# Kernel optimization log

Measured on AMD Instinct MI355X. Metric: run time of the kernel, lower is better.

The kernel has to match this reference:

```python
import jax, jax.numpy as jnp
import numpy as np

B, N, DIM = 4, 1024, 1024
HEADS, DIM_HEAD = 16, 64
ROT = 32
NUM_NULL = 2
EPS = 1e-5


def rotate_half(t):
    t1, t2 = jnp.split(t, 2, axis=-1)
    return jnp.concatenate((-t2, t1), axis=-1)


def apply_rope(t, freqs):
    # t: [..., n, rot]; freqs: [>=n, rot]
    f = freqs[-t.shape[-2]:, :]
    return t * jnp.cos(f) + rotate_half(t) * jnp.sin(f)


def layernorm(x, g, b):
    mu = jnp.mean(x, axis=-1, keepdims=True)
    var = jnp.var(x, axis=-1, keepdims=True)
    return (x - mu) * jax.lax.rsqrt(var + EPS) * g + b


def setup_inputs() -> dict:
    key = jax.random.key(0)
    ks = jax.random.split(key, 8)
    inner = HEADS * DIM_HEAD
    return {
        "x": jax.random.normal(ks[0], (B, N, DIM), jnp.float32),
        "mask": jnp.ones((B, N), dtype=bool),
        "freqs": jax.random.normal(ks[1], (N, ROT), jnp.float32),
        "ln_g": jnp.ones((DIM,), jnp.float32),
        "ln_b": jnp.zeros((DIM,), jnp.float32),
        "W_q": jax.random.normal(ks[2], (DIM, inner), jnp.float32) * (DIM ** -0.5),
        "W_kv": jax.random.normal(ks[3], (DIM, 2 * DIM_HEAD), jnp.float32) * (DIM ** -0.5),
        "W_out": jax.random.normal(ks[4], (inner, DIM), jnp.float32) * (inner ** -0.5),
        "null_kv": jax.random.normal(ks[5], (2, NUM_NULL, DIM_HEAD), jnp.float32),
    }


def reference(x, mask, freqs, ln_g, ln_b, W_q, W_kv, W_out, null_kv):
    b, n, _ = x.shape
    xn = layernorm(x, ln_g, ln_b)
    q = xn @ W_q                       # [b, n, h*d]
    kv = xn @ W_kv                     # [b, n, 2d]
    k, v = jnp.split(kv, 2, axis=-1)   # each [b, n, d] (multi-query)
    q = q.reshape(b, n, HEADS, DIM_HEAD).transpose(0, 2, 1, 3)  # [b, h, n, d]

    # partial rotary on first ROT dims of q, k, v (xpos_scale=None -> scale 1)
    ql, qr = q[..., :ROT], q[..., ROT:]
    kl, kr = k[..., :ROT], k[..., ROT:]
    vl, vr = v[..., :ROT], v[..., ROT:]
    q = jnp.concatenate((apply_rope(ql, freqs), qr), axis=-1)
    k = jnp.concatenate((apply_rope(kl, freqs), kr), axis=-1)
    v = jnp.concatenate((apply_rope(vl, freqs), vr), axis=-1)

    # prepend null k/v
    null_k = jnp.broadcast_to(null_kv[0], (b, NUM_NULL, DIM_HEAD))
    null_v = jnp.broadcast_to(null_kv[1], (b, NUM_NULL, DIM_HEAD))
    k = jnp.concatenate((null_k, k), axis=-2)  # [b, j, d]
    v = jnp.concatenate((null_v, v), axis=-2)
    m = jnp.concatenate((jnp.ones((b, NUM_NULL), bool), mask), axis=-1)  # [b, j]

    i, j = q.shape[-2], k.shape[-2]
    scale = DIM_HEAD ** -0.5
    sim = jnp.einsum('bhid,bjd->bhij', q, k) * scale
    neg = -jnp.finfo(sim.dtype).max
    sim = jnp.where(m[:, None, None, :], sim, neg)
    causal_mask = jnp.triu(jnp.ones((i, j), bool), k=j - i + 1)
    sim = jnp.where(causal_mask, neg, sim)
    attn = jax.nn.softmax(sim, axis=-1)
    out = jnp.einsum('bhij,bjd->bhid', attn, v)
    out = out.transpose(0, 2, 1, 3).reshape(b, n, HEADS * DIM_HEAD)
    return out @ W_out
```

## Files before the change

### kernel.cpp

```cpp
#include <hip/hip_runtime.h>
#include <hip/hip_bf16.h>

typedef __bf16 bf16;
typedef __bf16 bf16x8 __attribute__((ext_vector_type(8)));
typedef float  f32x4  __attribute__((ext_vector_type(4)));

#define SCL 0.18033688011112042f

__device__ __forceinline__ void gl2lds16(const bf16* g, bf16* l) {
    __builtin_amdgcn_global_load_lds(
        (const __attribute__((address_space(1))) unsigned int*)g,
        (__attribute__((address_space(3))) unsigned int*)l, 16, 0, 0);
}

__global__ __launch_bounds__(256) void setup_kernel(
    const float* __restrict__ x, const float* __restrict__ g, const float* __restrict__ b,
    bf16* __restrict__ xn, const float* __restrict__ W_q, const float* __restrict__ W_kv,
    const float* __restrict__ W_out, bf16* __restrict__ wcomb, bf16* __restrict__ wot,
    const float* __restrict__ freqs, const float* __restrict__ nullkv,
    float2* __restrict__ cs, bf16* __restrict__ knull, bf16* __restrict__ vtn) {
    int blk = blockIdx.x, t = threadIdx.x;
    if (blk < 4096) {
        int row = blk;
        float4 v = ((const float4*)(x + (size_t)row * 1024))[t];
        float f0 = v.x, f1 = v.y, f2 = v.z, f3 = v.w;
        float s  = f0 + f1 + f2 + f3;
        float ss = f0 * f0 + f1 * f1 + f2 * f2 + f3 * f3;
#pragma unroll
        for (int off = 32; off; off >>= 1) {
            s  += __shfl_xor(s, off);
            ss += __shfl_xor(ss, off);
        }
        __shared__ float rs[4], rss[4];
        int wave = t >> 6, lane = t & 63;
        if (lane == 0) { rs[wave] = s; rss[wave] = ss; }
        __syncthreads();
        s  = rs[0] + rs[1] + rs[2] + rs[3];
        ss = rss[0] + rss[1] + rss[2] + rss[3];
        float mu  = s * (1.0f / 1024.0f);
        float inv = rsqrtf(ss * (1.0f / 1024.0f) - mu * mu + 1e-5f);
        float4 gv = ((const float4*)g)[t], bv = ((const float4*)b)[t];
        float o0 = (f0 - mu) * inv * gv.x + bv.x;
        float o1 = (f1 - mu) * inv * gv.y + bv.y;
        float o2 = (f2 - mu) * inv * gv.z + bv.z;
        float o3 = (f3 - mu) * inv * gv.w + bv.w;
        __align__(8) bf16 ob[4] = {(bf16)o0, (bf16)o1, (bf16)o2, (bf16)o3};
        ((uint2*)(xn + (size_t)row * 1024))[t] = *(uint2*)ob;
    } else if (blk < 6272) {
        const float* src;
        bf16* dst;
        int R = 1024, C, bx, by;
        if (blk < 5120) {
            src = W_q; dst = wcomb; C = 1024;
            int i = blk - 4096; bx = i & 31; by = i >> 5;
        } else if (blk < 5248) {
            src = W_kv; dst = wcomb + 1024 * 1024; C = 128;
            int i = blk - 5120; bx = i & 3; by = i >> 2;
        } else {
            src = W_out; dst = wot; C = 1024;
            int i = blk - 5248; bx = i & 31; by = i >> 5;
        }
        __shared__ bf16 tile[32][33];
        int tx = t & 31, ty = t >> 5;
        int c0 = bx * 32, r0 = by * 32;
#pragma unroll
        for (int i = 0; i < 4; ++i)
            tile[ty + 8 * i][tx] = (bf16)src[(size_t)(r0 + ty + 8 * i) * C + c0 + tx];
        __syncthreads();
#pragma unroll
        for (int i = 0; i < 4; ++i)
            dst[(size_t)(c0 + ty + 8 * i) * R + r0 + tx] = tile[tx][ty + 8 * i];
    } else if (blk < 6400) {
        int idx = (blk - 6272) * 256 + t;
        float f = freqs[idx];
        cs[idx] = make_float2(cosf(f), sinf(f));
    } else if (blk == 6400) {
        for (int i = t; i < 4 * 62 * 64; i += 256) {
            int bb = i / (62 * 64), rem = i % (62 * 64);
            int r = rem / 64, d = rem % 64;
            knull[((size_t)bb * 1088 + 1026 + r) * 64 + d] = (bf16)0.f;
            vtn[((size_t)(bb * 64 + d)) * 1088 + 1026 + r] = (bf16)0.f;
        }
    } else {
        for (int i = t; i < 4 * 2 * 64; i += 256) {
            int bb = i / 128, rem = i % 128;
            int j = rem / 64, d = rem % 64;
            knull[((size_t)bb * 1088 + j) * 64 + d] = (bf16)(nullkv[j * 64 + d] * SCL);
            vtn[((size_t)(bb * 64 + d)) * 1088 + j] = (bf16)nullkv[128 + j * 64 + d];
        }
    }
}

template <int MODE, typename OutT>
__global__ __launch_bounds__(256) void gemm_glds(const bf16* __restrict__ A,
                                                 const bf16* __restrict__ Bt,
                                                 OutT* __restrict__ C, int K,
                                                 const float2* __restrict__ cs,
                                                 bf16* __restrict__ kout,
                                                 bf16* __restrict__ vout) {
    __shared__ __align__(16) bf16 As[64 * 64];
    __shared__ __align__(16) bf16 Bs[128 * 64];
    const int t = threadIdx.x;
    const int wave = t >> 6, lane = t & 63;
    const int wm = wave >> 1, wn = wave & 1;
    const int r16 = lane & 15, g = lane >> 4;
    const int m0 = blockIdx.x * 64, n0 = blockIdx.y * 128;

    int aRow[2], aOff[2], aLds[2], bRow[4], bOff[4], bLds[4];
#pragma unroll
    for (int j = 0; j < 2; ++j) {
        int c = t + 256 * j, row = c >> 3, p = c & 7;
        aRow[j] = row; aOff[j] = (p ^ (row & 7)) * 8; aLds[j] = c * 8;
    }
#pragma unroll
    for (int j = 0; j < 4; ++j) {
        int c = t + 256 * j, row = c >> 3, p = c & 7;
        bRow[j] = row; bOff[j] = (p ^ (row & 7)) * 8; bLds[j] = c * 8;
    }
    int offA[2][2], offB[2][4];
#pragma unroll
    for (int s = 0; s < 2; ++s) {
#pragma unroll
        for (int i = 0; i < 2; ++i) {
            int rA = wm * 32 + i * 16 + r16;
            offA[s][i] = rA * 64 + (((g + 4 * s) ^ (rA & 7)) * 8);
        }
#pragma unroll
        for (int i = 0; i < 4; ++i) {
            int rB = wn * 64 + i * 16 + r16;
            offB[s][i] = rB * 64 + (((g + 4 * s) ^ (rB & 7)) * 8);
        }
    }

    f32x4 acc[2][4] = {};
    for (int k0 = 0; k0 < K; k0 += 64) {
#pragma unroll
        for (int j = 0; j < 2; ++j)
            gl2lds16(A + (size_t)(m0 + aRow[j]) * K + k0 + aOff[j], As + aLds[j]);
#pragma unroll
        for (int j = 0; j < 4; ++j)
            gl2lds16(Bt + (size_t)(n0 + bRow[j]) * K + k0 + bOff[j], Bs + bLds[j]);
        __syncthreads();
#pragma unroll
        for (int s = 0; s < 2; ++s) {
            bf16x8 af[2], bfr[4];
#pragma unroll
            for (int mi = 0; mi < 2; ++mi) af[mi] = *(const bf16x8*)(As + offA[s][mi]);
#pragma unroll
            for (int ni = 0; ni < 4; ++ni) bfr[ni] = *(const bf16x8*)(Bs + offB[s][ni]);
#pragma unroll
            for (int mi = 0; mi < 2; ++mi)
#pragma unroll
                for (int ni = 0; ni < 4; ++ni)
                    acc[mi][ni] = __builtin_amdgcn_mfma_f32_16x16x32_bf16(
                        af[mi], bfr[ni], acc[mi][ni], 0, 0, 0);
        }
        __syncthreads();
    }
    if constexpr (MODE == 0) {
#pragma unroll
        for (int mi = 0; mi < 2; ++mi)
#pragma unroll
            for (int ni = 0; ni < 4; ++ni)
#pragma unroll
                for (int q2 = 0; q2 < 4; ++q2) {
                    int rr = m0 + wm * 32 + mi * 16 + g * 4 + q2;
                    int ccol = n0 + wn * 64 + ni * 16 + r16;
                    C[(size_t)rr * 1024 + ccol] = (OutT)acc[mi][ni][q2];
                }
    } else {
        bool isq = blockIdx.y < 8;
#pragma unroll
        for (int mi = 0; mi < 2; ++mi)
#pragma unroll
            for (int q2 = 0; q2 < 4; ++q2) {
                int rr = m0 + wm * 32 + mi * 16 + g * 4 + q2;
                int n = rr & 1023, bb = rr >> 10;
                const float2* csr = cs + n * 32;
                float2 c0 = csr[r16], c1 = csr[r16 + 16];
                float t0 = acc[mi][0][q2], t1 = acc[mi][1][q2];
                float t2 = acc[mi][2][q2], t3 = acc[mi][3][q2];
                float o0 = t0 * c0.x - t1 * c0.y;
                float o1 = t1 * c1.x + t0 * c1.y;
                if (isq) {
                    size_t rb = (size_t)rr * 1024 + n0 + wn * 64 + r16;
                    C[rb]      = (OutT)o0;
                    C[rb + 16] = (OutT)o1;
                    C[rb + 32] = (OutT)t2;
                    C[rb + 48] = (OutT)t3;
                } else {
                    if (wn == 0) {
                        bf16* kr = kout + ((size_t)bb * 1088 + n + 2) * 64 + r16;
                        kr[0]  = (bf16)(o0 * SCL);
                        kr[16] = (bf16)(o1 * SCL);
                        kr[32] = (bf16)(t2 * SCL);
                        kr[48] = (bf16)(t3 * SCL);
                    } else {
                        bf16* vr = vout + ((size_t)bb * 64 + r16) * 1088 + n + 2;
                        vr[0]         = (bf16)o0;
                        vr[16 * 1088] = (bf16)o1;
                        vr[32 * 1088] = (bf16)t2;
                        vr[48 * 1088] = (bf16)t3;
                    }
                }
            }
    }
}

__global__ __launch_bounds__(256) void attn_mfma(const bf16* __restrict__ knull,
                                                 const bf16* __restrict__ vtn,
                                                 const bf16* __restrict__ q,
                                                 bf16* __restrict__ out) {
    __shared__ __align__(16) bf16 k_s[2][64 * 64];
    __shared__ __align__(16) bf16 vt_s[2][64 * 64];
    __shared__ __align__(16) bf16 p_s[4][16 * 64];
    const int blk = blockIdx.x;
    const int qt = 15 - (blk >> 6);
    const int bh = blk & 63;
    const int b = bh >> 4, h = bh & 15;
    const int r0 = qt * 64;
    const int t = threadIdx.x, wave = t >> 6, lane = t & 63;
    const int lr = lane & 15, lg = lane >> 4;

    const int sj = t >> 3;
    const bf16* kgp = knull + ((size_t)b * 1088 + sj) * 64 + (t & 7) * 8;
    const bf16* vgp = vtn + ((size_t)(b * 64 + sj)) * 1088 + (t & 7) * 8;
    const int so0 = sj * 64 + (((t & 7) ^ (sj & 7)) * 8);
    const int so1 = so0 + 32 * 64;

#define ISSUE(K0, K1, V0, V1, KB) {                                   \
        int j0_ = (KB) * 64;                                          \
        K0 = *(const uint4*)(kgp + (size_t)j0_ * 64);                 \
        K1 = *(const uint4*)(kgp + (size_t)(j0_ + 32) * 64);          \
        V0 = *(const uint4*)(vgp + j0_);                              \
        V1 = *(const uint4*)(vgp + 32 * 1088 + j0_); }
#define COMMIT(BUF, K0, K1, V0, V1) {                                 \
        *(uint4*)(k_s[BUF] + so0) = K0; *(uint4*)(k_s[BUF] + so1) = K1; \
        *(uint4*)(vt_s[BUF] + so0) = V0; *(uint4*)(vt_s[BUF] + so1) = V1; }

    const int qrow = r0 + wave * 16 + lr;
    const bf16* qp = q + (size_t)(b * 1024 + qrow) * 1024 + h * 64;
    bf16x8 qf0 = *(const bf16x8*)(qp + lg * 8);
    bf16x8 qf1 = *(const bf16x8*)(qp + 32 + lg * 8);

    float m = -3.0e38f, l = 0.f;
    f32x4 O[4] = {};
    const int nkb = qt + 2;
    uint4 kA0, kA1, vA0, vA1, kB0, kB1, vB0, vB1;
    ISSUE(kA0, kA1, vA0, vA1, 0);

    for (int kb = 0; kb < nkb; ++kb) {
        if ((kb & 1) == 0) {
            COMMIT(0, kA0, kA1, vA0, vA1);
            if (kb + 1 < nkb) ISSUE(kB0, kB1, vB0, vB1, kb + 1);
        } else {
            COMMIT(1, kB0, kB1, vB0, vB1);
            if (kb + 1 < nkb) ISSUE(kA0, kA1, vA0, vA1, kb + 1);
        }
        __syncthreads();
        const bf16* ks = k_s[kb & 1];
        const bf16* vs = vt_s[kb & 1];

        if (kb * 64 <= r0 + wave * 16 + 17) {
            f32x4 sc[4];
#pragma unroll
            for (int kt = 0; kt < 4; ++kt) {
                int krow = kt * 16 + lr, sw = lr & 7;
                bf16x8 kf0 = *(const bf16x8*)(ks + krow * 64 + ((lg ^ sw) * 8));
                bf16x8 kf1 = *(const bf16x8*)(ks + krow * 64 + (((4 + lg) ^ sw) * 8));
                sc[kt] = __builtin_amdgcn_mfma_f32_16x16x32_bf16(
                    kf0, qf0, (f32x4){0.f, 0.f, 0.f, 0.f}, 0, 0, 0);
                sc[kt] = __builtin_amdgcn_mfma_f32_16x16x32_bf16(kf1, qf1, sc[kt], 0, 0, 0);
            }
            float pv_[4][4];
            float smax = -3.0e38f;
            bool domask = (kb * 64 + 63 > r0 + wave * 16 + 2);
            if (domask) {
#pragma unroll
                for (int kt = 0; kt < 4; ++kt)
#pragma unroll
                    for (int r = 0; r < 4; ++r) {
                        float s = sc[kt][r];
                        int gkey = kb * 64 + kt * 16 + lg * 4 + r;
                        if (gkey > qrow + 2) s = -3.0e38f;
                        pv_[kt][r] = s;
                        smax = fmaxf(smax, s);
                    }
            } else {
#pragma unroll
                for (int kt = 0; kt < 4; ++kt)
#pragma unroll
                    for (int r = 0; r < 4; ++r) {
                        float s = sc[kt][r];
                        pv_[kt][r] = s;
                        smax = fmaxf(smax, s);
                    }
            }
            smax = fmaxf(smax, __shfl_xor(smax, 16));
            smax = fmaxf(smax, __shfl_xor(smax, 32));
            float mnew = fmaxf(m, smax);
            float corr = exp2f(m - mnew);
            float ps = 0.f;
#pragma unroll
            for (int kt = 0; kt < 4; ++kt)
#pragma unroll
                for (int r = 0; r < 4; ++r) {
                    float p = exp2f(pv_[kt][r] - mnew);
                    pv_[kt][r] = p;
                    ps += p;
                }
            ps += __shfl_xor(ps, 16);
            ps += __shfl_xor(ps, 32);
            l = l * corr + ps;
            m = mnew;
            bf16* pw = p_s[wave];
#pragma unroll
            for (int kt = 0; kt < 4; ++kt) {
                __align__(8) bf16 pk[4] = {(bf16)pv_[kt][0], (bf16)pv_[kt][1],
                                           (bf16)pv_[kt][2], (bf16)pv_[kt][3]};
                int ch = (2 * kt + (lg >> 1)) ^ (lr & 7);
                *(uint2*)((char*)pw + lr * 128 + ch * 16 + (lg & 1) * 8) = *(const uint2*)pk;
            }
            asm volatile("" ::: "memory");
            float corr4[4];
#pragma unroll
            for (int r = 0; r < 4; ++r) corr4[r] = __shfl(corr, lg * 4 + r);
            bf16x8 af0 = *(const bf16x8*)(pw + lr * 64 + ((lg ^ (lr & 7)) * 8));
            bf16x8 af1 = *(const bf16x8*)(pw + lr * 64 + (((4 + lg) ^ (lr & 7)) * 8));
#pragma unroll
            for (int nt = 0; nt < 4; ++nt) {
#pragma unroll
                for (int r = 0; r < 4; ++r) O[nt][r] *= corr4[r];
                int vrow = nt * 16 + lr, sw = lr & 7;
                bf16x8 vf0 = *(const bf16x8*)(vs + vrow * 64 + ((lg ^ sw) * 8));
                bf16x8 vf1 = *(const bf16x8*)(vs + vrow * 64 + (((4 + lg) ^ sw) * 8));
                O[nt] = __builtin_amdgcn_mfma_f32_16x16x32_bf16(af0, vf0, O[nt], 0, 0, 0);
                O[nt] = __builtin_amdgcn_mfma_f32_16x16x32_bf16(af1, vf1, O[nt], 0, 0, 0);
            }
        }
    }
#undef ISSUE
#undef COMMIT
    float l4[4];
#pragma unroll
    for (int r = 0; r < 4; ++r) l4[r] = __shfl(l, lg * 4 + r);
#pragma unroll
    for (int nt = 0; nt < 4; ++nt)
#pragma unroll
        for (int r = 0; r < 4; ++r) {
            int qr = r0 + wave * 16 + 4 * lg + r;
            out[(size_t)(b * 1024 + qr) * 1024 + h * 64 + nt * 16 + lr] =
                (bf16)(O[nt][r] / l4[r]);
        }
}

extern "C" void kernel_launch(void* const* d_in, const int* in_sizes, int n_in,
                              void* d_out, int out_size, void* d_ws, size_t ws_size,
                              hipStream_t stream) {
    (void)out_size; (void)ws_size;
    const float *x = nullptr, *freqs = nullptr, *ln_g = nullptr, *ln_b = nullptr,
                *W_q = nullptr, *W_kv = nullptr, *W_out = nullptr, *nullkv = nullptr;
    for (int i = 0; i < n_in; ++i) {
        const float* p = (const float*)d_in[i];
        switch (in_sizes[i]) {
            case 4194304: if (!x) x = p; break;
            case 32768:   if (!freqs) freqs = p; break;
            case 1024:    if (!ln_g) ln_g = p; else ln_b = p; break;
            case 1048576: if (!W_q) W_q = p; else W_out = p; break;
            case 131072:  if (!W_kv) W_kv = p; break;
            case 256:     if (!nullkv) nullkv = p; break;
            default: break;
        }
    }

    char* ws = (char*)d_ws;
    bf16*   xn    = (bf16*)(ws);
    bf16*   qb    = (bf16*)(ws + 8388608);
    bf16*   wcomb = (bf16*)(ws + 16777216);
    bf16*   wot   = (bf16*)(ws + 19136512);
    bf16*   knull = (bf16*)(ws + 21233664);
    bf16*   vtn   = (bf16*)(ws + 21790720);
    float2* cs    = (float2*)(ws + 22347776);
    bf16*   ao    = xn;

    setup_kernel<<<6402, 256, 0, stream>>>(x, ln_g, ln_b, xn, W_q, W_kv, W_out,
                                           wcomb, wot, freqs, nullkv, cs, knull, vtn);
    gemm_glds<3, bf16><<<dim3(64, 9), 256, 0, stream>>>(xn, wcomb, qb, 1024, cs,
                                                        knull, vtn);
    attn_mfma<<<1024, 256, 0, stream>>>(knull, vtn, qb, ao);
    gemm_glds<0, float><<<dim3(64, 8), 256, 0, stream>>>(ao, wot, (float*)d_out, 1024,
                                                         nullptr, nullptr, nullptr);
}
```

Baseline: 91.27 us.

## Double-buffer GEMM LDS tiles and swizzle workgroup order for locality

The GEMM main loop now uses two LDS buffers: it issues the global-to-LDS loads for the next K tile before computing on the current one, so memory latency can overlap with MFMA work. The block index is also remapped with a stride-8 swizzle (hardcoded to 64 M-tiles) to change which tiles run concurrently, likely aiming at XCD/L2 locality. LDS use doubles, which can reduce occupancy. The remap assumes gridDim.x is 64 and the grid size is a multiple of 8.

New measurement: 93.69 us. +2.7%, slower.

```diff
diff --git a/kernel.cpp b/kernel.cpp
--- a/kernel.cpp
+++ b/kernel.cpp
@@ -98,13 +98,17 @@
                                                  const float2* __restrict__ cs,
                                                  bf16* __restrict__ kout,
                                                  bf16* __restrict__ vout) {
-    __shared__ __align__(16) bf16 As[64 * 64];
-    __shared__ __align__(16) bf16 Bs[128 * 64];
+    __shared__ __align__(16) bf16 As[2][64 * 64];
+    __shared__ __align__(16) bf16 Bs[2][128 * 64];
     const int t = threadIdx.x;
     const int wave = t >> 6, lane = t & 63;
     const int wm = wave >> 1, wn = wave & 1;
     const int r16 = lane & 15, g = lane >> 4;
-    const int m0 = blockIdx.x * 64, n0 = blockIdx.y * 128;
+    const int nwg = gridDim.x * gridDim.y;
+    const int orig = blockIdx.y * gridDim.x + blockIdx.x;
+    const int swz = (orig & 7) * (nwg >> 3) + (orig >> 3);
+    const int bx = swz & 63, by = swz >> 6;
+    const int m0 = bx * 64, n0 = by * 128;
 
     int aRow[2], aOff[2], aLds[2], bRow[4], bOff[4], bLds[4];
 #pragma unroll
@@ -132,22 +136,28 @@
         }
     }
 
+#define STAGE(BUF, KK) {                                                          \
+        _Pragma("unroll") for (int j = 0; j < 2; ++j)                             \
+            gl2lds16(A + (size_t)(m0 + aRow[j]) * K + (KK) + aOff[j],             \
+                     As[BUF] + aLds[j]);                                          \
+        _Pragma("unroll") for (int j = 0; j < 4; ++j)                             \
+            gl2lds16(Bt + (size_t)(n0 + bRow[j]) * K + (KK) + bOff[j],            \
+                     Bs[BUF] + bLds[j]); }
+
     f32x4 acc[2][4] = {};
-    for (int k0 = 0; k0 < K; k0 += 64) {
-#pragma unroll
-        for (int j = 0; j < 2; ++j)
-            gl2lds16(A + (size_t)(m0 + aRow[j]) * K + k0 + aOff[j], As + aLds[j]);
-#pragma unroll
-        for (int j = 0; j < 4; ++j)
-            gl2lds16(Bt + (size_t)(n0 + bRow[j]) * K + k0 + bOff[j], Bs + bLds[j]);
-        __syncthreads();
+    const int nt = K >> 6;
+    STAGE(0, 0);
+    __syncthreads();
+    for (int kt = 0; kt < nt; ++kt) {
+        const int cur = kt & 1;
+        if (kt + 1 < nt) STAGE(cur ^ 1, (kt + 1) << 6);
 #pragma unroll
         for (int s = 0; s < 2; ++s) {
             bf16x8 af[2], bfr[4];
 #pragma unroll
-            for (int mi = 0; mi < 2; ++mi) af[mi] = *(const bf16x8*)(As + offA[s][mi]);
-#pragma unroll
-            for (int ni = 0; ni < 4; ++ni) bfr[ni] = *(const bf16x8*)(Bs + offB[s][ni]);
+            for (int mi = 0; mi < 2; ++mi) af[mi] = *(const bf16x8*)(As[cur] + offA[s][mi]);
+#pragma unroll
+            for (int ni = 0; ni < 4; ++ni) bfr[ni] = *(const bf16x8*)(Bs[cur] + offB[s][ni]);
 #pragma unroll
             for (int mi = 0; mi < 2; ++mi)
 #pragma unroll
@@ -157,6 +167,8 @@
         }
         __syncthreads();
     }
+#undef STAGE
+
     if constexpr (MODE == 0) {
 #pragma unroll
         for (int mi = 0; mi < 2; ++mi)
@@ -169,7 +181,7 @@
                     C[(size_t)rr * 1024 + ccol] = (OutT)acc[mi][ni][q2];
                 }
     } else {
-        bool isq = blockIdx.y < 8;
+        bool isq = by < 8;
 #pragma unroll
         for (int mi = 0; mi < 2; ++mi)
 #pragma unroll
```
